# Kernel optimization log

Hardware: AMD Instinct MI355X
Metric: run time of the kernel (lower is better)

The kernel has to match this reference:

```python
import jax, jax.numpy as jnp
import numpy as np


def setup_inputs() -> dict:
    key = jax.random.key(0)
    ks = jax.random.split(key, 7)
    C, IC, H, W, B = 512, 256, 64, 64, 8
    N = H * W
    return {
        "x": jax.random.normal(ks[0], (B, C, H, W), dtype=jnp.float32),
        "w_phi": jax.random.normal(ks[1], (IC, C), dtype=jnp.float32) * 0.02,
        "w_theta": jax.random.normal(ks[2], (IC, C), dtype=jnp.float32) * 0.02,
        "w_g": jax.random.normal(ks[3], (IC, C), dtype=jnp.float32) * 0.02,
        "w_mask": jax.random.normal(ks[4], (C, IC), dtype=jnp.float32) * 0.02,
        "pos_embedding": jax.random.normal(ks[5], (1, N, N), dtype=jnp.float32),
        "pos_embedding_decoder": jax.random.normal(ks[6], (1, IC, H, W), dtype=jnp.float32),
    }


def reference(x, w_phi, w_theta, w_g, w_mask, pos_embedding, pos_embedding_decoder):
    b, c, h, w = x.shape
    n = h * w
    xf = x.reshape(b, c, n)  # [b, c, n]
    # 1x1 convs as channel matmuls
    phi = jnp.einsum('oc,bcn->bon', w_phi, xf)      # [b, ic, n]
    theta = jnp.einsum('oc,bcn->bon', w_theta, xf)  # [b, ic, n]
    g = jnp.einsum('oc,bcn->bon', w_g, xf) + pos_embedding_decoder.reshape(1, -1, n)
    g = jnp.swapaxes(g, 1, 2)  # [b, n, ic]
    # attention logits: theta^T @ phi -> [b, n_theta, n_phi], plus learned pos bias
    attn = jnp.einsum('bci,bcj->bij', theta, phi) + pos_embedding
    # NOTE: original softmax is over dim=1 (the theta/query axis), non-standard
    attn = jax.nn.softmax(attn, axis=1)
    y = jnp.einsum('bij,bjc->bic', attn, g)  # [b, n, ic]
    y = jnp.swapaxes(y, 1, 2).reshape(b, -1, n)  # [b, ic, n]
    mask = jnp.einsum('oc,bcn->bon', w_mask, y).reshape(b, c, h, w)
    return mask + x
```

## Files before the change

### kernel.cpp

```cpp
#include <hip/hip_runtime.h>

typedef short bf8 __attribute__((ext_vector_type(8)));
typedef float f32x4 __attribute__((ext_vector_type(4)));
typedef unsigned short us4 __attribute__((ext_vector_type(4)));
typedef unsigned short us8 __attribute__((ext_vector_type(8)));

#define DEVI __device__ __forceinline__

constexpr int NB = 8, NC = 512, NIC = 256, NS = 4096;

constexpr size_t OFF_XT  = 0;
constexpr size_t OFF_RS  = 0;
constexpr size_t OFF_TP  = 33554432;
constexpr size_t OFF_POS = 67108864;
constexpr size_t OFF_G   = 100663296;
constexpr size_t OFF_G2  = 117440512;
constexpr size_t OFF_Y   = 134217728;
constexpr size_t OFF_WTP = 150994944;
constexpr size_t OFF_WG  = 151519232;
constexpr size_t OFF_WM  = 151781376;
constexpr size_t OFF_E   = 152043520;
constexpr size_t E_END   = OFF_E + (size_t)268435456;

DEVI unsigned short f2bf(float f){
  unsigned u = __float_as_uint(f);
  u += 0x7fffu + ((u >> 16) & 1u);
  return (unsigned short)(u >> 16);
}
DEVI float bf2f(unsigned short b){ return __uint_as_float(((unsigned)b) << 16); }

DEVI void gld16(const void* g, void* l){
  __builtin_amdgcn_global_load_lds((const __attribute__((address_space(1))) unsigned int*)g,
                                   (__attribute__((address_space(3))) unsigned int*)l, 16, 0, 0);
}

DEVI void stageT(unsigned short* dst, const unsigned short* src, int ld, int wid, int lane){
  int rl = lane >> 3;
  int ce = ((lane & 7) << 3) ^ (rl << 3);
#pragma unroll
  for (int it = 0; it < 4; ++it){
    int q = wid + it * 4;
    gld16(src + (size_t)(q * 8 + rl) * ld + ce, dst + q * 512);
  }
}

DEVI void zero44(f32x4 (&a)[4][4]){
  f32x4 z = {0.f, 0.f, 0.f, 0.f};
#pragma unroll
  for (int i = 0; i < 4; ++i)
#pragma unroll
    for (int j = 0; j < 4; ++j) a[i][j] = z;
}

template<int NK64>
DEVI void gemm128v(const unsigned short* Ag, int lda, const unsigned short* Bg, int ldb,
                   unsigned short (&As)[2][8192], unsigned short (&Bs)[2][8192],
                   f32x4 (&acc)[4][4], int wid, int lane)
{
  const int wr = wid >> 1, wc = wid & 1;
  stageT(As[0], Ag, lda, wid, lane);
  stageT(Bs[0], Bg, ldb, wid, lane);
  __syncthreads();
  for (int kt = 0; kt < NK64; ++kt){
    int cur = kt & 1;
    if (kt + 1 < NK64){
      stageT(As[cur ^ 1], Ag + (kt + 1) * 64, lda, wid, lane);
      stageT(Bs[cur ^ 1], Bg + (kt + 1) * 64, ldb, wid, lane);
    }
    bf8 a[2][4], b[2][4];
#pragma unroll
    for (int ks = 0; ks < 2; ++ks){
      int cb = ks * 64 + ((lane >> 4) << 4);
#pragma unroll
      for (int f = 0; f < 4; ++f){
        int rA = wr * 64 + f * 16 + (lane & 15);
        a[ks][f] = *(const bf8*)((char*)As[cur] + rA * 128 + (cb ^ ((rA & 7) << 4)));
        int rB = wc * 64 + f * 16 + (lane & 15);
        b[ks][f] = *(const bf8*)((char*)Bs[cur] + rB * 128 + (cb ^ ((rB & 7) << 4)));
      }
    }
    __builtin_amdgcn_s_setprio(1);
#pragma unroll
    for (int ks = 0; ks < 2; ++ks)
#pragma unroll
      for (int i = 0; i < 4; ++i)
#pragma unroll
        for (int j = 0; j < 4; ++j)
          acc[i][j] = __builtin_amdgcn_mfma_f32_16x16x32_bf16(a[ks][i], b[ks][j], acc[i][j], 0, 0, 0);
    __builtin_amdgcn_s_setprio(0);
    __syncthreads();
  }
}


__global__ void k_prep(const float* wphi, const float* wtheta, const float* wgf, const float* wmf,
                       unsigned short* wtp, unsigned short* wgb, unsigned short* wmb){
  int idx = (blockIdx.x * 256 + threadIdx.x) * 4;
  const float* src; unsigned short* dst;
  if (idx < 131072)      { src = wphi + idx;            dst = wtp + idx; }
  else if (idx < 262144) { src = wtheta + (idx - 131072); dst = wtp + idx; }
  else if (idx < 393216) { src = wgf + (idx - 262144);  dst = wgb + (idx - 262144); }
  else                   { src = wmf + (idx - 393216);  dst = wmb + (idx - 393216); }
  f32x4 v = *(const f32x4*)src;
  us4 o;
#pragma unroll
  for (int r = 0; r < 4; ++r) o[r] = f2bf(v[r]);
  *(us4*)dst = o;
}

__global__ void k_pos(const float* pos, unsigned short* posb){
  size_t base = ((size_t)blockIdx.x * 256 + threadIdx.x) * 8;
  f32x4 v0 = *(const f32x4*)&pos[base];
  f32x4 v1 = *(const f32x4*)&pos[base + 4];
  us8 o;
#pragma unroll
  for (int r = 0; r < 4; ++r){ o[r] = f2bf(v0[r]); o[r + 4] = f2bf(v1[r]); }
  *(us8*)&posb[base] = o;
}

__global__ void k_xt(const float* x, unsigned short* xT){
  int b = blockIdx.z, ct = blockIdx.y, nt = blockIdx.x;
  __shared__ float t[64][65];
  int tid = threadIdx.x;
  int c0 = ct * 64, n0 = nt * 64;
  const float* xp = x + (size_t)b * NC * NS;
#pragma unroll
  for (int it = 0; it < 16; ++it){
    int idx = it * 256 + tid; int r = idx >> 6, cc = idx & 63;
    t[r][cc] = xp[(size_t)(c0 + r) * NS + n0 + cc];
  }
  __syncthreads();
  unsigned short* xo = xT + (size_t)b * NS * NC;
#pragma unroll
  for (int it = 0; it < 16; ++it){
    int idx = it * 256 + tid; int r = idx >> 6, cc = idx & 63;
    xo[(size_t)(n0 + r) * NC + c0 + cc] = f2bf(t[cc][r]);
  }
}


__global__ __launch_bounds__(256, 2) void k_tp(const unsigned short* wtp, const unsigned short* xT,
                                               unsigned short* tp){
  int b = blockIdx.z, ot = blockIdx.y, nt = blockIdx.x;
  int tid = threadIdx.x, wid = tid >> 6, lane = tid & 63, wr = wid >> 1, wc = wid & 1;
  __shared__ unsigned short As[2][8192], Bs[2][8192];
  f32x4 acc[4][4]; zero44(acc);
  gemm128v<8>(wtp + (size_t)(ot * 128) * 512, 512,
              xT + ((size_t)b * NS + nt * 128) * 512, 512, As, Bs, acc, wid, lane);
  unsigned short* out = tp + (size_t)b * NS * 512;
#pragma unroll
  for (int fr = 0; fr < 4; ++fr)
#pragma unroll
    for (int fc = 0; fc < 4; ++fc){
      int o0 = ot * 128 + wr * 64 + fr * 16 + ((lane >> 4) << 2);
      int n  = nt * 128 + wc * 64 + fc * 16 + (lane & 15);
      us4 v;
#pragma unroll
      for (int r = 0; r < 4; ++r) v[r] = f2bf(acc[fr][fc][r]);
      *(us4*)&out[(size_t)n * 512 + o0] = v;
    }
}

__global__ __launch_bounds__(256, 2) void k_g(const unsigned short* xT, const unsigned short* wgb,
                                              const float* pdec, unsigned short* gb){
  int b = blockIdx.z, ot = blockIdx.y, nt = blockIdx.x;
  int tid = threadIdx.x, wid = tid >> 6, lane = tid & 63, wr = wid >> 1, wc = wid & 1;
  __shared__ unsigned short As[2][8192], Bs[2][8192];
  f32x4 acc[4][4]; zero44(acc);
  gemm128v<8>(xT + ((size_t)b * NS + nt * 128) * 512, 512,
              wgb + (size_t)(ot * 128) * 512, 512, As, Bs, acc, wid, lane);
#pragma unroll
  for (int fr = 0; fr < 4; ++fr)
#pragma unroll
    for (int fc = 0; fc < 4; ++fc){
      int n0 = nt * 128 + wr * 64 + fr * 16 + ((lane >> 4) << 2);
      int o  = ot * 128 + wc * 64 + fc * 16 + (lane & 15);
      f32x4 pd = *(const f32x4*)&pdec[(size_t)o * NS + n0];
      us4 v;
#pragma unroll
      for (int r = 0; r < 4; ++r) v[r] = f2bf(acc[fr][fc][r] + pd[r]);
      *(us4*)&gb[((size_t)b * NIC + o) * NS + n0] = v;
    }
}

template<bool SE>
__global__ __launch_bounds__(256, 2) void k_statsE(const unsigned short* __restrict__ tp,
                                                   const unsigned short* __restrict__ posb,
                                                   float* __restrict__ rs,
                                                   unsigned short* __restrict__ E){
  int bid = blockIdx.x;
  int b = bid & 7, jb0 = (bid >> 3) * 64;
  int tid = threadIdx.x, wid = tid >> 6, lane = tid & 63;
  int p = wid >> 1, q = wid & 1, h = lane >> 4, l15 = lane & 15;
  __shared__ unsigned short Ath[4][8192];
  __shared__ float red[64];
  const unsigned short* tpb = tp + (size_t)b * NS * 512;
  unsigned short* Eb = SE ? (E + (size_t)b * NS * NS) : nullptr;

  bf8 bphi[8][2];
#pragma unroll
  for (int kb = 0; kb < 8; ++kb)
#pragma unroll
    for (int frj = 0; frj < 2; ++frj)
      bphi[kb][frj] = *(const bf8*)&tpb[(size_t)(jb0 + p * 32 + frj * 16 + l15) * 512
                                        + kb * 32 + h * 8];

  float sacc[2][4];
#pragma unroll
  for (int a = 0; a < 2; ++a)
#pragma unroll
    for (int r = 0; r < 4; ++r) sacc[a][r] = 0.f;

  stageT(Ath[0], tpb + 256, 512, wid, lane);
  stageT(Ath[1], tpb + 256 + 64, 512, wid, lane);

  for (int it = 0; it < 32; ++it){
    int i0t = it * 128;
    const unsigned short* thBase = tpb + (size_t)i0t * 512 + 256;
    const unsigned short* thNext = tpb + (size_t)(it < 31 ? i0t + 128 : i0t) * 512 + 256;
    us4 pv[2][4];
#pragma unroll
    for (int frj = 0; frj < 2; ++frj)
#pragma unroll
      for (int fci = 0; fci < 4; ++fci){
        int iG = i0t + q * 64 + fci * 16 + l15;
        int jG = jb0 + p * 32 + frj * 16 + h * 4;
        pv[frj][fci] = *(const us4*)&posb[(size_t)iG * NS + jG];
      }
    f32x4 lacc[2][4];
    {
      f32x4 z = {0.f, 0.f, 0.f, 0.f};
#pragma unroll
      for (int a = 0; a < 2; ++a)
#pragma unroll
        for (int c = 0; c < 4; ++c) lacc[a][c] = z;
    }
#pragma unroll
    for (int ph = 0; ph < 4; ++ph){
      const unsigned short* ssrc = (ph < 2) ? thBase + (ph + 2) * 64 : thNext + (ph - 2) * 64;
      stageT(Ath[(ph + 2) & 3], ssrc, 512, wid, lane);
      if (ph < 2) asm volatile("s_waitcnt vmcnt(16)" ::: "memory");
      else        asm volatile("s_waitcnt vmcnt(8)"  ::: "memory");
      __builtin_amdgcn_s_barrier();
      __builtin_amdgcn_sched_barrier(0);
#pragma unroll
      for (int ks = 0; ks < 2; ++ks){
        bf8 tfr[4];
#pragma unroll
        for (int fci = 0; fci < 4; ++fci){
          int rI = q * 64 + fci * 16 + l15;
          int cbyte = (ks * 64 + (h << 4)) ^ ((rI & 7) << 4);
          tfr[fci] = *(const bf8*)((char*)Ath[ph] + rI * 128 + cbyte);
        }
        __builtin_amdgcn_s_setprio(1);
#pragma unroll
        for (int frj = 0; frj < 2; ++frj)
#pragma unroll
          for (int fci = 0; fci < 4; ++fci)
            lacc[frj][fci] = __builtin_amdgcn_mfma_f32_16x16x32_bf16(bphi[ph * 2 + ks][frj], tfr[fci],
                                                                     lacc[frj][fci], 0, 0, 0);
        __builtin_amdgcn_s_setprio(0);
      }
    }
#pragma unroll
    for (int frj = 0; frj < 2; ++frj)
#pragma unroll
      for (int fci = 0; fci < 4; ++fci){
        us4 ev;
#pragma unroll
        for (int r = 0; r < 4; ++r){
          float e = __expf(lacc[frj][fci][r] + bf2f(pv[frj][fci][r]));
          sacc[frj][r] += e;
          if (SE) ev[r] = f2bf(e);
        }
        if (SE){
          int iG = i0t + q * 64 + fci * 16 + l15;
          int jG = jb0 + p * 32 + frj * 16 + h * 4;
          *(us4*)&Eb[(size_t)iG * NS + jG] = ev;
        }
      }
  }
#pragma unroll
  for (int m = 1; m <= 8; m <<= 1)
#pragma unroll
    for (int frj = 0; frj < 2; ++frj)
#pragma unroll
      for (int r = 0; r < 4; ++r)
        sacc[frj][r] += __shfl_xor(sacc[frj][r], m, 64);
  if (q == 0 && l15 == 0){
#pragma unroll
    for (int frj = 0; frj < 2; ++frj)
#pragma unroll
      for (int r = 0; r < 4; ++r)
        red[p * 32 + frj * 16 + h * 4 + r] = sacc[frj][r];
  }
  __syncthreads();
  if (q == 1 && l15 == 0){
#pragma unroll
    for (int frj = 0; frj < 2; ++frj)
#pragma unroll
      for (int r = 0; r < 4; ++r){
        int jl = p * 32 + frj * 16 + h * 4 + r;
        float s = sacc[frj][r] + red[jl];
        rs[(size_t)b * NS + jb0 + jl] = 1.f / s;
      }
  }
}

__global__ void k_sg(const unsigned short* gb, const float* rs, unsigned short* g2){
  size_t base = ((size_t)blockIdx.x * 256 + threadIdx.x) * 8;
  int b = (int)(base / ((size_t)NIC * NS));
  int j0 = (int)(base % NS);
  const float* rsb = rs + (size_t)b * NS + j0;
  f32x4 r0 = *(const f32x4*)&rsb[0];
  f32x4 r1 = *(const f32x4*)&rsb[4];
  us8 gv = *(const us8*)&gb[base];
  us8 o;
#pragma unroll
  for (int r = 0; r < 4; ++r){
    o[r]     = f2bf(bf2f(gv[r])     * r0[r]);
    o[r + 4] = f2bf(bf2f(gv[r + 4]) * r1[r]);
  }
  *(us8*)&g2[base] = o;
}

__global__ __launch_bounds__(256, 2) void k_yg(const unsigned short* __restrict__ g2,
                                               const unsigned short* __restrict__ E,
                                               unsigned short* __restrict__ yb){
  int b = blockIdx.z, ct = blockIdx.y, nt = blockIdx.x;
  int tid = threadIdx.x, wid = tid >> 6, lane = tid & 63, wr = wid >> 1, wc = wid & 1;
  __shared__ unsigned short As[2][8192], Bs[2][8192];
  f32x4 acc[4][4]; zero44(acc);
  gemm128v<64>(g2 + ((size_t)b * NIC + ct * 128) * NS, NS,
               E + ((size_t)b * NS + nt * 128) * NS, NS, As, Bs, acc, wid, lane);
  unsigned short* yo = yb + (size_t)b * NS * NIC;
#pragma unroll
  for (int fr = 0; fr < 4; ++fr)
#pragma unroll
    for (int fc = 0; fc < 4; ++fc){
      int c0 = ct * 128 + wr * 64 + fr * 16 + ((lane >> 4) << 2);
      int i  = nt * 128 + wc * 64 + fc * 16 + (lane & 15);
      us4 v;
#pragma unroll
      for (int r = 0; r < 4; ++r) v[r] = f2bf(acc[fr][fc][r]);
      *(us4*)&yo[(size_t)i * NIC + c0] = v;
    }
}

__global__ __launch_bounds__(256, 2) void k_y(const unsigned short* __restrict__ tp,
                                              const unsigned short* __restrict__ posb,
                                              const unsigned short* __restrict__ g2,
                                              unsigned short* __restrict__ yb){
  int bid = blockIdx.x;
  int b = bid & 7, i0 = (bid >> 3) * 64;
  int tid = threadIdx.x, wid = tid >> 6, lane = tid & 63;
  int p = wid >> 1, q = wid & 1;
  __shared__ unsigned short Aph[4][8192];
  __shared__ unsigned short El[64 * 128];
  const unsigned short* tpb = tp + (size_t)b * NS * 512;

  bf8 btr[8][2];
#pragma unroll
  for (int kb = 0; kb < 8; ++kb)
#pragma unroll
    for (int fc = 0; fc < 2; ++fc)
      btr[kb][fc] = *(const bf8*)&tpb[(size_t)(i0 + p * 32 + fc * 16 + (lane & 15)) * 512
                                      + 256 + kb * 32 + (lane >> 4) * 8];

  f32x4 yacc[4][4]; zero44(yacc);
  stageT(Aph[0], tpb, 512, wid, lane);
  stageT(Aph[1], tpb + 64, 512, wid, lane);

  const unsigned short* g2b = g2 + (size_t)b * NIC * NS;

  for (int jt = 0; jt < 32; ++jt){
    int j0 = jt * 128;
    const unsigned short* phiBase = tpb + (size_t)j0 * 512;
    const unsigned short* phiNext = tpb + (size_t)(jt < 31 ? j0 + 128 : j0) * 512;
    us4 pv[4][2];
#pragma unroll
    for (int fr = 0; fr < 4; ++fr){
      int jl = q * 64 + fr * 16 + ((lane >> 4) << 2);
#pragma unroll
      for (int fc = 0; fc < 2; ++fc){
        int il = p * 32 + fc * 16 + (lane & 15);
        pv[fr][fc] = *(const us4*)&posb[(size_t)(i0 + il) * NS + j0 + jl];
      }
    }
    f32x4 lacc[4][2];
    {
      f32x4 z = {0.f, 0.f, 0.f, 0.f};
#pragma unroll
      for (int i = 0; i < 4; ++i)
#pragma unroll
        for (int j = 0; j < 2; ++j) lacc[i][j] = z;
    }
#pragma unroll
    for (int ph = 0; ph < 4; ++ph){
      const unsigned short* ssrc = (ph < 2) ? phiBase + (ph + 2) * 64 : phiNext + (ph - 2) * 64;
      stageT(Aph[(ph + 2) & 3], ssrc, 512, wid, lane);
      if (ph < 2) asm volatile("s_waitcnt vmcnt(16)" ::: "memory");
      else        asm volatile("s_waitcnt vmcnt(8)"  ::: "memory");
      __builtin_amdgcn_s_barrier();
      __builtin_amdgcn_sched_barrier(0);
#pragma unroll
      for (int ks = 0; ks < 2; ++ks){
        bf8 a[4];
#pragma unroll
        for (int fr = 0; fr < 4; ++fr){
          int r = q * 64 + fr * 16 + (lane & 15);
          int cbyte = (ks * 64 + ((lane >> 4) << 4)) ^ ((r & 7) << 4);
          a[fr] = *(const bf8*)((char*)Aph[ph] + r * 128 + cbyte);
        }
        __builtin_amdgcn_s_setprio(1);
#pragma unroll
        for (int fr = 0; fr < 4; ++fr)
#pragma unroll
          for (int fc = 0; fc < 2; ++fc)
            lacc[fr][fc] = __builtin_amdgcn_mfma_f32_16x16x32_bf16(a[fr], btr[ph * 2 + ks][fc],
                                                                   lacc[fr][fc], 0, 0, 0);
        __builtin_amdgcn_s_setprio(0);
      }
    }
#pragma unroll
    for (int fr = 0; fr < 4; ++fr)
#pragma unroll
      for (int fc = 0; fc < 2; ++fc){
        int il = p * 32 + fc * 16 + (lane & 15);
        int jl = q * 64 + fr * 16 + ((lane >> 4) << 2);
        us4 ev;
#pragma unroll
        for (int r = 0; r < 4; ++r)
          ev[r] = f2bf(__expf(lacc[fr][fc][r] + bf2f(pv[fr][fc][r])));
        *(us4*)((char*)El + il * 256 + ((jl * 2) ^ ((il & 7) << 4))) = ev;
      }
    __builtin_amdgcn_sched_barrier(0);
    asm volatile("s_waitcnt lgkmcnt(0)" ::: "memory");
    __builtin_amdgcn_s_barrier();
    __builtin_amdgcn_sched_barrier(0);
#pragma unroll
    for (int jk = 0; jk < 4; ++jk){
      bf8 eb[4];
#pragma unroll
      for (int f = 0; f < 4; ++f){
        int ei = f * 16 + (lane & 15);
        int ebt = jk * 64 + ((lane >> 4) << 4);
        eb[f] = *(const bf8*)((char*)El + ei * 256 + (ebt ^ ((ei & 7) << 4)));
      }
      __builtin_amdgcn_s_setprio(1);
#pragma unroll
      for (int cf = 0; cf < 4; ++cf){
        int c = wid * 64 + cf * 16 + (lane & 15);
        bf8 ga = *(const bf8*)&g2b[(size_t)c * NS + j0 + jk * 32 + (lane >> 4) * 8];
#pragma unroll
        for (int f = 0; f < 4; ++f)
          yacc[cf][f] = __builtin_amdgcn_mfma_f32_16x16x32_bf16(ga, eb[f], yacc[cf][f], 0, 0, 0);
      }
      __builtin_amdgcn_s_setprio(0);
    }
  }
  unsigned short* yo = yb + (size_t)b * NS * NIC;
#pragma unroll
  for (int cf = 0; cf < 4; ++cf)
#pragma unroll
    for (int f = 0; f < 4; ++f){
      int c0 = wid * 64 + cf * 16 + ((lane >> 4) << 2);
      int ig = i0 + f * 16 + (lane & 15);
      us4 v;
#pragma unroll
      for (int r = 0; r < 4; ++r) v[r] = f2bf(yacc[cf][f][r]);
      *(us4*)&yo[(size_t)ig * NIC + c0] = v;
    }
}

__global__ __launch_bounds__(256, 2) void k_out(const unsigned short* yb, const unsigned short* wmb,
                                                const float* xg, float* outg){
  int b = blockIdx.z, cot = blockIdx.y, nt = blockIdx.x;
  int tid = threadIdx.x, wid = tid >> 6, lane = tid & 63, wr = wid >> 1, wc = wid & 1;
  __shared__ unsigned short As[2][8192], Bs[2][8192];
  f32x4 acc[4][4]; zero44(acc);
  gemm128v<4>(yb + ((size_t)b * NS + nt * 128) * 256, 256,
              wmb + (size_t)(cot * 128) * 256, 256, As, Bs, acc, wid, lane);
#pragma unroll
  for (int fr = 0; fr < 4; ++fr)
#pragma unroll
    for (int fc = 0; fc < 4; ++fc){
      int n0 = nt * 128 + wr * 64 + fr * 16 + ((lane >> 4) << 2);
      int co = cot * 128 + wc * 64 + fc * 16 + (lane & 15);
      f32x4 xv = *(const f32x4*)&xg[((size_t)b * NC + co) * NS + n0];
      f32x4 ov = acc[fr][fc] + xv;
      *(f32x4*)&outg[((size_t)b * NC + co) * NS + n0] = ov;
    }
}

extern "C" void kernel_launch(void* const* d_in, const int* in_sizes, int n_in,
                              void* d_out, int out_size, void* d_ws, size_t ws_size,
                              hipStream_t stream){
  const float* x      = (const float*)d_in[0];
  const float* wphi   = (const float*)d_in[1];
  const float* wtheta = (const float*)d_in[2];
  const float* wgf    = (const float*)d_in[3];
  const float* wmf    = (const float*)d_in[4];
  const float* pos    = (const float*)d_in[5];
  const float* pdec   = (const float*)d_in[6];
  float* outg = (float*)d_out;
  char* ws = (char*)d_ws;
  unsigned short* xT   = (unsigned short*)(ws + OFF_XT);
  float*          rsv  = (float*)(ws + OFF_RS);
  unsigned short* tp   = (unsigned short*)(ws + OFF_TP);
  unsigned short* posb = (unsigned short*)(ws + OFF_POS);
  unsigned short* gb   = (unsigned short*)(ws + OFF_G);
  unsigned short* g2   = (unsigned short*)(ws + OFF_G2);
  unsigned short* yb   = (unsigned short*)(ws + OFF_Y);
  unsigned short* wtp  = (unsigned short*)(ws + OFF_WTP);
  unsigned short* wgb  = (unsigned short*)(ws + OFF_WG);
  unsigned short* wmb  = (unsigned short*)(ws + OFF_WM);
  unsigned short* Ebuf = (unsigned short*)(ws + OFF_E);

  bool epath = (ws_size >= E_END);

  k_prep<<<512, 256, 0, stream>>>(wphi, wtheta, wgf, wmf, wtp, wgb, wmb);
  k_pos<<<8192, 256, 0, stream>>>(pos, posb);
  k_xt<<<dim3(64, 8, 8), 256, 0, stream>>>(x, xT);
  k_tp<<<dim3(32, 4, 8), 256, 0, stream>>>(wtp, xT, tp);
  k_g<<<dim3(32, 2, 8), 256, 0, stream>>>(xT, wgb, pdec, gb);

  if (epath){
    k_statsE<true><<<512, 256, 0, stream>>>(tp, posb, rsv, Ebuf);
    k_sg<<<4096, 256, 0, stream>>>(gb, rsv, g2);
    k_yg<<<dim3(32, 2, 8), 256, 0, stream>>>(g2, Ebuf, yb);
  } else {
    k_statsE<false><<<512, 256, 0, stream>>>(tp, posb, rsv, nullptr);
    k_sg<<<4096, 256, 0, stream>>>(gb, rsv, g2);
    k_y<<<512, 256, 0, stream>>>(tp, posb, g2, yb);
  }
  k_out<<<dim3(32, 4, 8), 256, 0, stream>>>(yb, wmb, x, outg);
}
```

Baseline: 485.8 us.

## Chunk the softmax numerator over key blocks so the E buffer stays cache-resident

Result: slower. 512.9 us (+5.6%).

```diff
diff --git a/kernel.cpp b/kernel.cpp
--- a/kernel.cpp
+++ b/kernel.cpp
@@ -11,6 +11,7 @@
 
 constexpr size_t OFF_XT  = 0;
 constexpr size_t OFF_RS  = 0;
+constexpr size_t OFF_SP  = 262144;
 constexpr size_t OFF_TP  = 33554432;
 constexpr size_t OFF_POS = 67108864;
 constexpr size_t OFF_G   = 100663296;
@@ -19,8 +20,9 @@
 constexpr size_t OFF_WTP = 150994944;
 constexpr size_t OFF_WG  = 151519232;
 constexpr size_t OFF_WM  = 151781376;
-constexpr size_t OFF_E   = 152043520;
-constexpr size_t E_END   = OFF_E + (size_t)268435456;
+constexpr size_t OFF_YF  = 152043520;
+constexpr size_t OFF_E   = 185597952;
+constexpr size_t E_END   = OFF_E + (size_t)67108864;
 
 DEVI unsigned short f2bf(float f){
   unsigned u = __float_as_uint(f);
@@ -183,11 +185,199 @@
     }
 }
 
-template<bool SE>
-__global__ __launch_bounds__(256, 2) void k_statsE(const unsigned short* __restrict__ tp,
+__global__ __launch_bounds__(256, 2) void k_statsC(const unsigned short* __restrict__ tp,
                                                    const unsigned short* __restrict__ posb,
-                                                   float* __restrict__ rs,
-                                                   unsigned short* __restrict__ E){
+                                                   float* __restrict__ sp,
+                                                   unsigned short* __restrict__ E,
+                                                   int j0c){
+  int bid = blockIdx.x;
+  int b = bid & 7;
+  int jblk = (bid >> 3) & 15, ih = bid >> 7;
+  int jb0 = j0c + jblk * 64;
+  int tid = threadIdx.x, wid = tid >> 6, lane = tid & 63;
+  int p = wid >> 1, q = wid & 1, h = lane >> 4, l15 = lane & 15;
+  __shared__ unsigned short Ath[4][8192];
+  __shared__ float red[64];
+  const unsigned short* tpb = tp + (size_t)b * NS * 512;
+  unsigned short* Eb = E + (size_t)b * NS * 1024;
+
+  bf8 bphi[8][2];
+#pragma unroll
+  for (int kb = 0; kb < 8; ++kb)
+#pragma unroll
+    for (int frj = 0; frj < 2; ++frj)
+      bphi[kb][frj] = *(const bf8*)&tpb[(size_t)(jb0 + p * 32 + frj * 16 + l15) * 512
+                                        + kb * 32 + h * 8];
+
+  float sacc[2][4];
+#pragma unroll
+  for (int a = 0; a < 2; ++a)
+#pragma unroll
+    for (int r = 0; r < 4; ++r) sacc[a][r] = 0.f;
+
+  int it0 = ih * 8;
+  stageT(Ath[0], tpb + (size_t)(it0 * 128) * 512 + 256, 512, wid, lane);
+  stageT(Ath[1], tpb + (size_t)(it0 * 128) * 512 + 256 + 64, 512, wid, lane);
+
+  for (int it = it0; it < it0 + 8; ++it){
+    int i0t = it * 128;
+    const unsigned short* thBase = tpb + (size_t)i0t * 512 + 256;
+    const unsigned short* thNext = tpb + (size_t)((it < it0 + 7) ? i0t + 128 : i0t) * 512 + 256;
+    us4 pv[2][4];
+#pragma unroll
+    for (int frj = 0; frj < 2; ++frj)
+#pragma unroll
+      for (int fci = 0; fci < 4; ++fci){
+        int iG = i0t + q * 64 + fci * 16 + l15;
+        int jG = jb0 + p * 32 + frj * 16 + h * 4;
+        pv[frj][fci] = *(const us4*)&posb[(size_t)iG * NS + jG];
+      }
+    f32x4 lacc[2][4];
+    {
+      f32x4 z = {0.f, 0.f, 0.f, 0.f};
+#pragma unroll
+      for (int a = 0; a < 2; ++a)
+#pragma unroll
+        for (int c = 0; c < 4; ++c) lacc[a][c] = z;
+    }
+#pragma unroll
+    for (int ph = 0; ph < 4; ++ph){
+      const unsigned short* ssrc = (ph < 2) ? thBase + (ph + 2) * 64 : thNext + (ph - 2) * 64;
+      stageT(Ath[(ph + 2) & 3], ssrc, 512, wid, lane);
+      if (ph < 2) asm volatile("s_waitcnt vmcnt(16)" ::: "memory");
+      else        asm volatile("s_waitcnt vmcnt(8)"  ::: "memory");
+      __builtin_amdgcn_s_barrier();
+      __builtin_amdgcn_sched_barrier(0);
+#pragma unroll
+      for (int ks = 0; ks < 2; ++ks){
+        bf8 tfr[4];
+#pragma unroll
+        for (int fci = 0; fci < 4; ++fci){
+          int rI = q * 64 + fci * 16 + l15;
+          int cbyte = (ks * 64 + (h << 4)) ^ ((rI & 7) << 4);
+          tfr[fci] = *(const bf8*)((char*)Ath[ph] + rI * 128 + cbyte);
+        }
+        __builtin_amdgcn_s_setprio(1);
+#pragma unroll
+        for (int frj = 0; frj < 2; ++frj)
+#pragma unroll
+          for (int fci = 0; fci < 4; ++fci)
+            lacc[frj][fci] = __builtin_amdgcn_mfma_f32_16x16x32_bf16(bphi[ph * 2 + ks][frj], tfr[fci],
+                                                                     lacc[frj][fci], 0, 0, 0);
+        __builtin_amdgcn_s_setprio(0);
+      }
+    }
+#pragma unroll
+    for (int frj = 0; frj < 2; ++frj)
+#pragma unroll
+      for (int fci = 0; fci < 4; ++fci){
+        us4 ev;
+#pragma unroll
+        for (int r = 0; r < 4; ++r){
+          float e = __expf(lacc[frj][fci][r] + bf2f(pv[frj][fci][r]));
+          sacc[frj][r] += e;
+          ev[r] = f2bf(e);
+        }
+        int iG = i0t + q * 64 + fci * 16 + l15;
+        int jloc = jblk * 64 + p * 32 + frj * 16 + h * 4;
+        *(us4*)&Eb[(size_t)iG * 1024 + jloc] = ev;
+      }
+  }
+#pragma unroll
+  for (int m = 1; m <= 8; m <<= 1)
+#pragma unroll
+    for (int frj = 0; frj < 2; ++frj)
+#pragma unroll
+      for (int r = 0; r < 4; ++r)
+        sacc[frj][r] += __shfl_xor(sacc[frj][r], m, 64);
+  if (q == 0 && l15 == 0){
+#pragma unroll
+    for (int frj = 0; frj < 2; ++frj)
+#pragma unroll
+      for (int r = 0; r < 4; ++r)
+        red[p * 32 + frj * 16 + h * 4 + r] = sacc[frj][r];
+  }
+  __syncthreads();
+  if (q == 1 && l15 == 0){
+#pragma unroll
+    for (int frj = 0; frj < 2; ++frj)
+#pragma unroll
+      for (int r = 0; r < 4; ++r){
+        int jl = p * 32 + frj * 16 + h * 4 + r;
+        float s = sacc[frj][r] + red[jl];
+        sp[(size_t)(ih * 8 + b) * NS + jb0 + jl] = s;
+      }
+  }
+}
+
+__global__ void k_rs4(const float* sp, float* rs, int j0c){
+  int idx = blockIdx.x * 256 + threadIdx.x;
+  int b = idx >> 10, jj = idx & 1023;
+  int j = j0c + jj;
+  float s = 0.f;
+#pragma unroll
+  for (int ih = 0; ih < 4; ++ih) s += sp[(size_t)(ih * 8 + b) * NS + j];
+  rs[(size_t)b * NS + j] = 1.f / s;
+}
+
+__global__ void k_sg(const unsigned short* gb, const float* rs, unsigned short* g2,
+                     int j0c, int chjsh){
+  size_t t8 = ((size_t)blockIdx.x * 256 + threadIdx.x) * 8;
+  int CHJm1 = (1 << chjsh) - 1;
+  int b  = (int)(t8 >> (8 + chjsh));
+  int o  = (int)((t8 >> chjsh) & 255);
+  int jj = (int)(t8 & CHJm1);
+  size_t base = ((size_t)(b * 256 + o)) * NS + j0c + jj;
+  const float* rsb = rs + (size_t)b * NS + j0c + jj;
+  f32x4 r0 = *(const f32x4*)&rsb[0];
+  f32x4 r1 = *(const f32x4*)&rsb[4];
+  us8 gv = *(const us8*)&gb[base];
+  us8 o8;
+#pragma unroll
+  for (int r = 0; r < 4; ++r){
+    o8[r]     = f2bf(bf2f(gv[r])     * r0[r]);
+    o8[r + 4] = f2bf(bf2f(gv[r + 4]) * r1[r]);
+  }
+  *(us8*)&g2[base] = o8;
+}
+
+__global__ __launch_bounds__(256, 2) void k_yg(const unsigned short* __restrict__ g2,
+                                               const unsigned short* __restrict__ E,
+                                               float* __restrict__ yf, int j0c, int accum){
+  int b = blockIdx.z, ct = blockIdx.y, nt = blockIdx.x;
+  int tid = threadIdx.x, wid = tid >> 6, lane = tid & 63, wr = wid >> 1, wc = wid & 1;
+  __shared__ unsigned short As[2][8192], Bs[2][8192];
+  f32x4 acc[4][4]; zero44(acc);
+  gemm128v<16>(g2 + ((size_t)b * NIC + ct * 128) * NS + j0c, NS,
+               E + ((size_t)b * NS + nt * 128) * 1024, 1024, As, Bs, acc, wid, lane);
+  float* yo = yf + (size_t)b * NS * NIC;
+#pragma unroll
+  for (int fr = 0; fr < 4; ++fr)
+#pragma unroll
+    for (int fc = 0; fc < 4; ++fc){
+      int c0 = ct * 128 + wr * 64 + fr * 16 + ((lane >> 4) << 2);
+      int i  = nt * 128 + wc * 64 + fc * 16 + (lane & 15);
+      float* dst = &yo[(size_t)i * NIC + c0];
+      f32x4 v = acc[fr][fc];
+      if (accum) v = v + *(const f32x4*)dst;
+      *(f32x4*)dst = v;
+    }
+}
+
+__global__ void k_cvt(const float* yf, unsigned short* yb){
+  size_t base = ((size_t)blockIdx.x * 256 + threadIdx.x) * 8;
+  f32x4 v0 = *(const f32x4*)&yf[base];
+  f32x4 v1 = *(const f32x4*)&yf[base + 4];
+  us8 o;
+#pragma unroll
+  for (int r = 0; r < 4; ++r){ o[r] = f2bf(v0[r]); o[r + 4] = f2bf(v1[r]); }
+  *(us8*)&yb[base] = o;
+}
+
+
+__global__ __launch_bounds__(256, 2) void k_stats(const unsigned short* __restrict__ tp,
+                                                  const unsigned short* __restrict__ posb,
+                                                  float* __restrict__ rs){
   int bid = blockIdx.x;
   int b = bid & 7, jb0 = (bid >> 3) * 64;
   int tid = threadIdx.x, wid = tid >> 6, lane = tid & 63;
@@ -195,7 +385,6 @@
   __shared__ unsigned short Ath[4][8192];
   __shared__ float red[64];
   const unsigned short* tpb = tp + (size_t)b * NS * 512;
-  unsigned short* Eb = SE ? (E + (size_t)b * NS * NS) : nullptr;
 
   bf8 bphi[8][2];
 #pragma unroll
@@ -204,7 +393,6 @@
     for (int frj = 0; frj < 2; ++frj)
       bphi[kb][frj] = *(const bf8*)&tpb[(size_t)(jb0 + p * 32 + frj * 16 + l15) * 512
                                         + kb * 32 + h * 8];
-
   float sacc[2][4];
 #pragma unroll
   for (int a = 0; a < 2; ++a)
@@ -265,20 +453,10 @@
 #pragma unroll
     for (int frj = 0; frj < 2; ++frj)
 #pragma unroll
-      for (int fci = 0; fci < 4; ++fci){
-        us4 ev;
-#pragma unroll
-        for (int r = 0; r < 4; ++r){
-          float e = __expf(lacc[frj][fci][r] + bf2f(pv[frj][fci][r]));
-          sacc[frj][r] += e;
-          if (SE) ev[r] = f2bf(e);
-        }
-        if (SE){
-          int iG = i0t + q * 64 + fci * 16 + l15;
-          int jG = jb0 + p * 32 + frj * 16 + h * 4;
-          *(us4*)&Eb[(size_t)iG * NS + jG] = ev;
-        }
-      }
+      for (int fci = 0; fci < 4; ++fci)
+#pragma unroll
+        for (int r = 0; r < 4; ++r)
+          sacc[frj][r] += __expf(lacc[frj][fci][r] + bf2f(pv[frj][fci][r]));
   }
 #pragma unroll
   for (int m = 1; m <= 8; m <<= 1)
@@ -305,46 +483,6 @@
         rs[(size_t)b * NS + jb0 + jl] = 1.f / s;
       }
   }
-}
-
-__global__ void k_sg(const unsigned short* gb, const float* rs, unsigned short* g2){
-  size_t base = ((size_t)blockIdx.x * 256 + threadIdx.x) * 8;
-  int b = (int)(base / ((size_t)NIC * NS));
-  int j0 = (int)(base % NS);
-  const float* rsb = rs + (size_t)b * NS + j0;
-  f32x4 r0 = *(const f32x4*)&rsb[0];
-  f32x4 r1 = *(const f32x4*)&rsb[4];
-  us8 gv = *(const us8*)&gb[base];
-  us8 o;
-#pragma unroll
-  for (int r = 0; r < 4; ++r){
-    o[r]     = f2bf(bf2f(gv[r])     * r0[r]);
-    o[r + 4] = f2bf(bf2f(gv[r + 4]) * r1[r]);
-  }
-  *(us8*)&g2[base] = o;
-}
-
-__global__ __launch_bounds__(256, 2) void k_yg(const unsigned short* __restrict__ g2,
-                                               const unsigned short* __restrict__ E,
-                                               unsigned short* __restrict__ yb){
-  int b = blockIdx.z, ct = blockIdx.y, nt = blockIdx.x;
-  int tid = threadIdx.x, wid = tid >> 6, lane = tid & 63, wr = wid >> 1, wc = wid & 1;
-  __shared__ unsigned short As[2][8192], Bs[2][8192];
-  f32x4 acc[4][4]; zero44(acc);
-  gemm128v<64>(g2 + ((size_t)b * NIC + ct * 128) * NS, NS,
-               E + ((size_t)b * NS + nt * 128) * NS, NS, As, Bs, acc, wid, lane);
-  unsigned short* yo = yb + (size_t)b * NS * NIC;
-#pragma unroll
-  for (int fr = 0; fr < 4; ++fr)
-#pragma unroll
-    for (int fc = 0; fc < 4; ++fc){
-      int c0 = ct * 128 + wr * 64 + fr * 16 + ((lane >> 4) << 2);
-      int i  = nt * 128 + wc * 64 + fc * 16 + (lane & 15);
-      us4 v;
-#pragma unroll
-      for (int r = 0; r < 4; ++r) v[r] = f2bf(acc[fr][fc][r]);
-      *(us4*)&yo[(size_t)i * NIC + c0] = v;
-    }
 }
 
 __global__ __launch_bounds__(256, 2) void k_y(const unsigned short* __restrict__ tp,
@@ -507,6 +645,7 @@
   char* ws = (char*)d_ws;
   unsigned short* xT   = (unsigned short*)(ws + OFF_XT);
   float*          rsv  = (float*)(ws + OFF_RS);
+  float*          spv  = (float*)(ws + OFF_SP);
   unsigned short* tp   = (unsigned short*)(ws + OFF_TP);
   unsigned short* posb = (unsigned short*)(ws + OFF_POS);
   unsigned short* gb   = (unsigned short*)(ws + OFF_G);
@@ -515,6 +654,7 @@
   unsigned short* wtp  = (unsigned short*)(ws + OFF_WTP);
   unsigned short* wgb  = (unsigned short*)(ws + OFF_WG);
   unsigned short* wmb  = (unsigned short*)(ws + OFF_WM);
+  float*          yf   = (float*)(ws + OFF_YF);
   unsigned short* Ebuf = (unsigned short*)(ws + OFF_E);
 
   bool epath = (ws_size >= E_END);
@@ -526,12 +666,17 @@
   k_g<<<dim3(32, 2, 8), 256, 0, stream>>>(xT, wgb, pdec, gb);
 
   if (epath){
-    k_statsE<true><<<512, 256, 0, stream>>>(tp, posb, rsv, Ebuf);
-    k_sg<<<4096, 256, 0, stream>>>(gb, rsv, g2);
-    k_yg<<<dim3(32, 2, 8), 256, 0, stream>>>(g2, Ebuf, yb);
+    for (int c = 0; c < 4; ++c){
+      int j0c = c * 1024;
+      k_statsC<<<512, 256, 0, stream>>>(tp, posb, spv, Ebuf, j0c);
+      k_rs4<<<32, 256, 0, stream>>>(spv, rsv, j0c);
+      k_sg<<<1024, 256, 0, stream>>>(gb, rsv, g2, j0c, 10);
+      k_yg<<<dim3(32, 2, 8), 256, 0, stream>>>(g2, Ebuf, yf, j0c, c > 0 ? 1 : 0);
+    }
+    k_cvt<<<4096, 256, 0, stream>>>(yf, yb);
   } else {
-    k_statsE<false><<<512, 256, 0, stream>>>(tp, posb, rsv, nullptr);
-    k_sg<<<4096, 256, 0, stream>>>(gb, rsv, g2);
+    k_stats<<<512, 256, 0, stream>>>(tp, posb, rsv);
+    k_sg<<<4096, 256, 0, stream>>>(gb, rsv, g2, 0, 12);
     k_y<<<512, 256, 0, stream>>>(tp, posb, g2, yb);
   }
   k_out<<<dim3(32, 4, 8), 256, 0, stream>>>(yb, wmb, x, outg);
```
